# Kernel optimization log

Hardware: AMD Instinct MI355X
Metric: run time of the kernel (lower is better)

The kernel has to match this reference:

```python
import jax, jax.numpy as jnp
import numpy as np

B, S, D, K = 8, 4096, 256, 8192
BETA = 0.25


def setup_inputs() -> dict:
    key = jax.random.key(0)
    k1, k2 = jax.random.split(key)
    return {
        "z": jax.random.normal(k1, (B, S, D), dtype=jnp.float32),
        "embed": jax.random.normal(k2, (K, D), dtype=jnp.float32),
    }


def reference(z, embed):
    # Inference-path VQ-EMA forward (EMA buffer updates are a no-grad side
    # effect only active in training mode; excluded from the pure reference).
    num_codes, dim = embed.shape
    z_flat = z.reshape(-1, dim)                      # [N, D]
    # squared-euclidean distances: ||z||^2 - 2 z.e^T + ||e||^2  -> [N, K]
    dist = ((z_flat * z_flat).sum(1, keepdims=True)
            - 2.0 * (z_flat @ embed.T)
            + (embed * embed).sum(1)[None, :])
    idx = jnp.argmin(dist, axis=1)                   # [N]
    z_q = embed[idx].reshape(z.shape)                # gather instead of onehot @ embed
    # commitment loss: beta * mse(stop_grad(z_q), z)
    loss = BETA * jnp.mean(jnp.square(jax.lax.stop_gradient(z_q) - z))
    # straight-through estimator
    z_q_st = z + jax.lax.stop_gradient(z_q - z)
    # perplexity from code usage histogram (scatter-add instead of onehot.mean)
    counts = jnp.zeros((num_codes,), dtype=z.dtype).at[idx].add(1.0)
    avg_probs = counts / idx.shape[0]
    perplexity = jnp.exp(-jnp.sum(avg_probs * jnp.log(avg_probs + 1e-12)))
    return z_q_st, loss, perplexity, idx.reshape(z.shape[:-1])
```

## Files before the change

### kernel.cpp

```cpp
#include <hip/hip_runtime.h>
#include <stdint.h>
#include <math.h>

#define NROWS 32768
#define DIM   256
#define KCODES 8192
#define BETA  0.25f
#define CSPLIT 4
#define RSPLIT 16
#define NELEM 8388608
#define TAU 0.09375f

typedef float f32x4 __attribute__((ext_vector_type(4)));
typedef _Float16 v8h __attribute__((ext_vector_type(8)));
typedef unsigned short us4 __attribute__((ext_vector_type(4)));

__device__ inline unsigned int split1(float x) {
    _Float16 hf = (_Float16)x;
    _Float16 lf = (_Float16)(x - (float)hf);
    unsigned int h = __builtin_bit_cast(unsigned short, hf);
    unsigned int l = __builtin_bit_cast(unsigned short, lf);
    return h | (l << 16);
}

__device__ inline void gload_lds16(const void* g, void* l) {
    __builtin_amdgcn_global_load_lds(
        (const __attribute__((address_space(1))) void*)g,
        (__attribute__((address_space(3))) void*)l,
        16, 0, 0);
}

__device__ inline unsigned int fkey(float f) {
    unsigned int b = __float_as_uint(f);
    return (b & 0x80000000u) ? ~b : (b | 0x80000000u);
}

__global__ void prep_z(const float* __restrict__ z,
                       unsigned short* __restrict__ zhi,
                       unsigned short* __restrict__ zlo) {
    int t = blockIdx.x * blockDim.x + threadIdx.x;
    float4 v = reinterpret_cast<const float4*>(z)[t];
    unsigned int p0 = split1(v.x);
    unsigned int p1 = split1(v.y);
    unsigned int p2 = split1(v.z);
    unsigned int p3 = split1(v.w);
    us4 h, l;
    h[0] = (unsigned short)p0; l[0] = (unsigned short)(p0 >> 16);
    h[1] = (unsigned short)p1; l[1] = (unsigned short)(p1 >> 16);
    h[2] = (unsigned short)p2; l[2] = (unsigned short)(p2 >> 16);
    h[3] = (unsigned short)p3; l[3] = (unsigned short)(p3 >> 16);
    reinterpret_cast<us4*>(zhi)[t] = h;
    reinterpret_cast<us4*>(zlo)[t] = l;
}

__global__ void prep_e(const float* __restrict__ e,
                       unsigned short* __restrict__ ehi,
                       unsigned short* __restrict__ elo,
                       float* __restrict__ enrm) {
    int row = blockIdx.x;
    int d = threadIdx.x;
    float x = e[(size_t)row * DIM + d];
    unsigned int p = split1(x);
    ehi[(size_t)row * DIM + d] = (unsigned short)p;
    elo[(size_t)row * DIM + d] = (unsigned short)(p >> 16);
    float sq = x * x;
    #pragma unroll
    for (int off = 32; off; off >>= 1) sq += __shfl_down(sq, off);
    __shared__ float ps[4];
    if ((threadIdx.x & 63) == 0) ps[threadIdx.x >> 6] = sq;
    __syncthreads();
    if (threadIdx.x == 0) enrm[row] = 0.5f * (ps[0] + ps[1] + ps[2] + ps[3]);
}

__launch_bounds__(256, 2)
__global__ void gemm_hi(const unsigned short* __restrict__ zhi,
                        const unsigned short* __restrict__ ehi,
                        const float* __restrict__ enrm,
                        float* __restrict__ pval1,
                        int* __restrict__ pcol1,
                        float* __restrict__ pval2) {
    __shared__ __align__(16) unsigned short As[128 * 64];
    __shared__ __align__(16) unsigned short Bs[128 * 64];
    __shared__ float rv[2][128];
    __shared__ int   rc[2][128];
    __shared__ float rv2[2][128];

    const int tid = threadIdx.x;
    const int w = tid >> 6, l = tid & 63;
    const int lx = l & 15, quad = l >> 4;
    const int wm = w >> 1, wn = w & 1;
    const int arow_base = blockIdx.x * 128;
    const int cs = blockIdx.y;
    const int cbase_cs = cs * (KCODES / CSPLIT);

    float runv[16], runv2[16];
    int runc[16];
    #pragma unroll
    for (int s = 0; s < 16; ++s) {
        runv[s] = 3.0e38f; runv2[s] = 3.0e38f; runc[s] = 0x7fffffff;
    }

    const int st_row8 = l >> 3;
    const int st_g = (((l & 7) ^ (l >> 3)) * 8);
    const int fr_lx7 = lx & 7;

    for (int nt = 0; nt < (KCODES / CSPLIT) / 128; ++nt) {
        const int colbase = cbase_cs + nt * 128;
        f32x4 acc[4][4];
        #pragma unroll
        for (int mi = 0; mi < 4; ++mi)
            #pragma unroll
            for (int ni = 0; ni < 4; ++ni) {
                f32x4 zz = {0.f, 0.f, 0.f, 0.f};
                acc[mi][ni] = zz;
            }

        for (int bk = 0; bk < 4; ++bk) {
            const int ao = bk * 64;
            __syncthreads();
            #pragma unroll
            for (int j = 0; j < 4; ++j) {
                const int r = w * 32 + j * 8 + st_row8;
                gload_lds16(zhi + (size_t)(arow_base + r) * DIM + ao + st_g,
                            &As[(w * 32 + j * 8) * 64]);
                gload_lds16(ehi + (size_t)(colbase + r) * DIM + ao + st_g,
                            &Bs[(w * 32 + j * 8) * 64]);
            }
            __syncthreads();

            #pragma unroll
            for (int kc = 0; kc < 2; ++kc) {
                const int gsw = ((kc * 4 + quad) ^ fr_lx7) * 8;
                v8h af[4], bfr[4];
                #pragma unroll
                for (int mi = 0; mi < 4; ++mi)
                    af[mi] = *(const v8h*)&As[(wm * 64 + mi * 16 + lx) * 64 + gsw];
                #pragma unroll
                for (int ni = 0; ni < 4; ++ni)
                    bfr[ni] = *(const v8h*)&Bs[(wn * 64 + ni * 16 + lx) * 64 + gsw];
                #pragma unroll
                for (int mi = 0; mi < 4; ++mi)
                    #pragma unroll
                    for (int ni = 0; ni < 4; ++ni)
                        acc[mi][ni] = __builtin_amdgcn_mfma_f32_16x16x32_f16(
                            af[mi], bfr[ni], acc[mi][ni], 0, 0, 0);
            }
        }

        #pragma unroll
        for (int ni = 0; ni < 4; ++ni) {
            const int col = colbase + wn * 64 + ni * 16 + lx;
            const float es = enrm[col];
            #pragma unroll
            for (int mi = 0; mi < 4; ++mi)
                #pragma unroll
                for (int r = 0; r < 4; ++r) {
                    const int s = mi * 4 + r;
                    float sv = es - acc[mi][ni][r];
                    bool lt1 = sv < runv[s];
                    bool lt2 = sv < runv2[s];
                    float old1 = runv[s];
                    runv2[s] = lt1 ? old1 : (lt2 ? sv : runv2[s]);
                    runv[s] = lt1 ? sv : old1;
                    runc[s] = lt1 ? col : runc[s];
                }
        }
    }

    #pragma unroll
    for (int s = 0; s < 16; ++s) {
        float v1 = runv[s], v2 = runv2[s];
        int c1 = runc[s];
        #pragma unroll
        for (int m = 1; m < 16; m <<= 1) {
            float ov1 = __shfl_xor(v1, m);
            int oc1 = __shfl_xor(c1, m);
            float ov2 = __shfl_xor(v2, m);
            float mx = fmaxf(v1, ov1);
            v2 = fminf(fminf(v2, ov2), mx);
            bool take = (ov1 < v1) || (ov1 == v1 && oc1 < c1);
            v1 = take ? ov1 : v1;
            c1 = take ? oc1 : c1;
        }
        if (lx == 0) {
            const int mi = s >> 2, r = s & 3;
            const int rl = wm * 64 + mi * 16 + quad * 4 + r;
            rv[wn][rl] = v1; rc[wn][rl] = c1; rv2[wn][rl] = v2;
        }
    }
    __syncthreads();
    if (tid < 128) {
        float v1 = rv[0][tid], v2 = rv2[0][tid];
        int c1 = rc[0][tid];
        float ov1 = rv[1][tid], ov2 = rv2[1][tid];
        int oc1 = rc[1][tid];
        float mx = fmaxf(v1, ov1);
        v2 = fminf(fminf(v2, ov2), mx);
        bool take = (ov1 < v1) || (ov1 == v1 && oc1 < c1);
        v1 = take ? ov1 : v1;
        c1 = take ? oc1 : c1;
        const size_t row = (size_t)arow_base + tid;
        pval1[row * CSPLIT + cs] = v1;
        pcol1[row * CSPLIT + cs] = c1;
        pval2[row * CSPLIT + cs] = v2;
    }
}

__global__ void merge_flag(const float* __restrict__ pval1,
                           const int* __restrict__ pcol1,
                           const float* __restrict__ pval2,
                           int* __restrict__ colidx,
                           float* __restrict__ out_idx,
                           int* __restrict__ flagcnt,
                           int* __restrict__ flaglist) {
    int row = blockIdx.x * blockDim.x + threadIdx.x;
    float v1 = pval1[row * CSPLIT], v2 = pval2[row * CSPLIT];
    int c1 = pcol1[row * CSPLIT];
    #pragma unroll
    for (int cs = 1; cs < CSPLIT; ++cs) {
        float ov1 = pval1[row * CSPLIT + cs], ov2 = pval2[row * CSPLIT + cs];
        int oc1 = pcol1[row * CSPLIT + cs];
        float mx = fmaxf(v1, ov1);
        v2 = fminf(fminf(v2, ov2), mx);
        if (ov1 < v1 || (ov1 == v1 && oc1 < c1)) { v1 = ov1; c1 = oc1; }
    }
    colidx[row] = c1;
    out_idx[row] = (float)c1;
    if (v2 - v1 < TAU) {
        int slot = atomicAdd(flagcnt, 1);
        flaglist[slot] = row;
    }
}

__launch_bounds__(256, 2)
__global__ void rescue_gemm(const unsigned short* __restrict__ zhi,
                            const unsigned short* __restrict__ zlo,
                            const unsigned short* __restrict__ ehi,
                            const unsigned short* __restrict__ elo,
                            const float* __restrict__ enrm,
                            const int* __restrict__ flagcnt,
                            const int* __restrict__ flaglist,
                            unsigned long long* __restrict__ rkey) {
    __shared__ __align__(16) unsigned short As[128 * 64];
    __shared__ __align__(16) unsigned short Bs[128 * 64];
    __shared__ float rv[2][128];
    __shared__ int   rc[2][128];

    const int count = *flagcnt;
    const int tid = threadIdx.x;
    const int w = tid >> 6, l = tid & 63;
    const int lx = l & 15, quad = l >> 4;
    const int wm = w >> 1, wn = w & 1;
    const int cs = blockIdx.y;
    const int cbase_cs = cs * (KCODES / RSPLIT);

    const int st_row8 = l >> 3;
    const int st_g = (((l & 7) ^ (l >> 3)) * 8);
    const int fr_lx7 = lx & 7;

    for (int tb = blockIdx.x * 128; tb < count; tb += 32 * 128) {
        int arowj[4];
        #pragma unroll
        for (int j = 0; j < 4; ++j) {
            int li = tb + w * 32 + j * 8 + st_row8;
            arowj[j] = (li < count) ? flaglist[li] : 0;
        }

        float runv[16];
        int runc[16];
        #pragma unroll
        for (int s = 0; s < 16; ++s) { runv[s] = 3.0e38f; runc[s] = 0x7fffffff; }

        for (int nt = 0; nt < (KCODES / RSPLIT) / 128; ++nt) {
            const int colbase = cbase_cs + nt * 128;
            f32x4 acc[4][4];
            #pragma unroll
            for (int mi = 0; mi < 4; ++mi)
                #pragma unroll
                for (int ni = 0; ni < 4; ++ni) {
                    f32x4 zz = {0.f, 0.f, 0.f, 0.f};
                    acc[mi][ni] = zz;
                }

            #pragma unroll
            for (int seg = 0; seg < 3; ++seg) {
                const unsigned short* za = (seg == 2) ? zlo : zhi;
                const unsigned short* eb = (seg == 1) ? elo : ehi;
                for (int bk = 0; bk < 4; ++bk) {
                    const int ao = bk * 64;
                    __syncthreads();
                    #pragma unroll
                    for (int j = 0; j < 4; ++j) {
                        const int r = w * 32 + j * 8 + st_row8;
                        gload_lds16(za + (size_t)arowj[j] * DIM + ao + st_g,
                                    &As[(w * 32 + j * 8) * 64]);
                        gload_lds16(eb + (size_t)(colbase + r) * DIM + ao + st_g,
                                    &Bs[(w * 32 + j * 8) * 64]);
                    }
                    __syncthreads();
                    #pragma unroll
                    for (int kc = 0; kc < 2; ++kc) {
                        const int gsw = ((kc * 4 + quad) ^ fr_lx7) * 8;
                        v8h af[4], bfr[4];
                        #pragma unroll
                        for (int mi = 0; mi < 4; ++mi)
                            af[mi] = *(const v8h*)&As[(wm * 64 + mi * 16 + lx) * 64 + gsw];
                        #pragma unroll
                        for (int ni = 0; ni < 4; ++ni)
                            bfr[ni] = *(const v8h*)&Bs[(wn * 64 + ni * 16 + lx) * 64 + gsw];
                        #pragma unroll
                        for (int mi = 0; mi < 4; ++mi)
                            #pragma unroll
                            for (int ni = 0; ni < 4; ++ni)
                                acc[mi][ni] = __builtin_amdgcn_mfma_f32_16x16x32_f16(
                                    af[mi], bfr[ni], acc[mi][ni], 0, 0, 0);
                    }
                }
            }

            #pragma unroll
            for (int ni = 0; ni < 4; ++ni) {
                const int col = colbase + wn * 64 + ni * 16 + lx;
                const float es = enrm[col];
                #pragma unroll
                for (int mi = 0; mi < 4; ++mi)
                    #pragma unroll
                    for (int r = 0; r < 4; ++r) {
                        float sv = es - acc[mi][ni][r];
                        const int s = mi * 4 + r;
                        if (sv < runv[s]) { runv[s] = sv; runc[s] = col; }
                    }
            }
        }

        #pragma unroll
        for (int s = 0; s < 16; ++s) {
            float v = runv[s]; int c = runc[s];
            #pragma unroll
            for (int m = 1; m < 16; m <<= 1) {
                float ov = __shfl_xor(v, m);
                int oc = __shfl_xor(c, m);
                if (ov < v || (ov == v && oc < c)) { v = ov; c = oc; }
            }
            if (lx == 0) {
                const int mi = s >> 2, r = s & 3;
                const int rl = wm * 64 + mi * 16 + quad * 4 + r;
                rv[wn][rl] = v; rc[wn][rl] = c;
            }
        }
        __syncthreads();
        if (tid < 128) {
            float v0 = rv[0][tid]; int c0 = rc[0][tid];
            float v1 = rv[1][tid]; int c1 = rc[1][tid];
            if (v1 < v0 || (v1 == v0 && c1 < c0)) { v0 = v1; c0 = c1; }
            const int li = tb + tid;
            if (li < count) {
                unsigned long long key =
                    ((unsigned long long)fkey(v0) << 32) | (unsigned int)c0;
                atomicMin(&rkey[li], key);
            }
        }
        __syncthreads();
    }
}

__global__ void rescue_write(const unsigned long long* __restrict__ rkey,
                             const int* __restrict__ flagcnt,
                             const int* __restrict__ flaglist,
                             int* __restrict__ colidx,
                             float* __restrict__ out_idx) {
    int i = blockIdx.x * blockDim.x + threadIdx.x;
    if (i >= *flagcnt) return;
    int row = flaglist[i];
    int col = (int)(unsigned int)(rkey[i] & 0xFFFFFFFFull);
    colidx[row] = col;
    out_idx[row] = (float)col;
}

__global__ void fused_out(const int* __restrict__ colidx,
                          const float* __restrict__ z,
                          const float* __restrict__ embed,
                          float* __restrict__ out_zq,
                          float* __restrict__ counts,
                          float* __restrict__ lossAcc) {
    __shared__ int cidx[16];
    const int tid = threadIdx.x;
    if (tid < 16) {
        const int row = blockIdx.x * 16 + tid;
        const int c = colidx[row];
        cidx[tid] = c;
        atomicAdd(&counts[c], 1.0f);
    }
    __syncthreads();
    const int d = tid;
    float ls = 0.f;
    #pragma unroll 4
    for (int i = 0; i < 16; ++i) {
        const int row = blockIdx.x * 16 + i;
        const int c = cidx[i];
        const float zv = z[(size_t)row * DIM + d];
        const float ev = embed[(size_t)c * DIM + d];
        const float diff = ev - zv;
        out_zq[(size_t)row * DIM + d] = zv + diff;
        ls += diff * diff;
    }
    #pragma unroll
    for (int off = 32; off; off >>= 1) ls += __shfl_down(ls, off);
    __shared__ float ps[4];
    if ((tid & 63) == 0) ps[tid >> 6] = ls;
    __syncthreads();
    if (tid == 0) atomicAdd(lossAcc, ps[0] + ps[1] + ps[2] + ps[3]);
}

__global__ void finalize(const float* __restrict__ counts,
                         const float* __restrict__ lossAcc,
                         float* __restrict__ out_loss,
                         float* __restrict__ out_perp) {
    float h = 0.f;
    for (int k = threadIdx.x; k < KCODES; k += 256) {
        float p = counts[k] * (1.0f / (float)NROWS);
        h += p * logf(p + 1e-12f);
    }
    #pragma unroll
    for (int off = 32; off; off >>= 1) h += __shfl_down(h, off);
    __shared__ float ps[4];
    if ((threadIdx.x & 63) == 0) ps[threadIdx.x >> 6] = h;
    __syncthreads();
    if (threadIdx.x == 0) {
        *out_perp = expf(-(ps[0] + ps[1] + ps[2] + ps[3]));
        *out_loss = BETA * lossAcc[0] / (float)NELEM;
    }
}

extern "C" void kernel_launch(void* const* d_in, const int* in_sizes, int n_in,
                              void* d_out, int out_size, void* d_ws, size_t ws_size,
                              hipStream_t stream) {
    const float* z = (const float*)d_in[0];
    const float* embed = (const float*)d_in[1];
    char* ws = (char*)d_ws;

    unsigned short* zhi = (unsigned short*)(ws + 0);
    unsigned short* zlo = (unsigned short*)(ws + 16777216);
    unsigned short* ehi = (unsigned short*)(ws + 33554432);
    unsigned short* elo = (unsigned short*)(ws + 37748736);
    float* enrm    = (float*)(ws + 41943040);
    float* pval1   = (float*)(ws + 41975808);
    int*   pcol1   = (int*)  (ws + 42500096);
    float* pval2   = (float*)(ws + 43024384);
    int*   colidx  = (int*)  (ws + 43548672);
    float* counts  = (float*)(ws + 43679744);
    float* lossAcc = (float*)(ws + 43712512);
    int*   flagcnt = (int*)  (ws + 43712516);
    int*   flaglist = (int*) (ws + 43712520);
    unsigned long long* rkey = (unsigned long long*)(ws + 43843592);

    float* out = (float*)d_out;
    float* out_zq   = out;
    float* out_loss = out + 8388608;
    float* out_perp = out + 8388609;
    float* out_idx  = out + 8388610;

    (void)hipMemsetAsync(counts, 0, KCODES * 4 + 8, stream);
    (void)hipMemsetAsync(rkey, 0xFF, NROWS * 8, stream);

    prep_z<<<NELEM / 4 / 256, 256, 0, stream>>>(z, zhi, zlo);
    prep_e<<<KCODES, 256, 0, stream>>>(embed, ehi, elo, enrm);
    gemm_hi<<<dim3(NROWS / 128, CSPLIT), 256, 0, stream>>>(
        zhi, ehi, enrm, pval1, pcol1, pval2);
    merge_flag<<<NROWS / 256, 256, 0, stream>>>(
        pval1, pcol1, pval2, colidx, out_idx, flagcnt, flaglist);
    rescue_gemm<<<dim3(32, RSPLIT), 256, 0, stream>>>(
        zhi, zlo, ehi, elo, enrm, flagcnt, flaglist, rkey);
    rescue_write<<<NROWS / 256, 256, 0, stream>>>(
        rkey, flagcnt, flaglist, colidx, out_idx);
    fused_out<<<NROWS / 16, 256, 0, stream>>>(colidx, z, embed,
                                              out_zq, counts, lossAcc);
    finalize<<<1, 256, 0, stream>>>(counts, lossAcc, out_loss, out_perp);
}
```

Measured before the change: 387.0 us.

## Merge prep kernels, drop memsets and rescue_write, use med3 for top-2 tracking

Fuses prep_z and prep_e into one launch that also zeroes counts, the loss accumulator and the flag counter, which removes both memsets. rkey is now initialised per flagged slot in merge_flag, and flagged rows store a negative slot reference in colidx. fused_out resolves that reference, so the separate rescue_write kernel goes away. The top-2 update in gemm_hi uses fmed3/fminf instead of selects to cut VALU work in the inner epilogue. The hot epilogue's tie handling changes slightly, since fminf and the strict less-than comparison are used together.

```diff
diff --git a/kernel.cpp b/kernel.cpp
--- a/kernel.cpp
+++ b/kernel.cpp
@@ -35,41 +35,49 @@
     return (b & 0x80000000u) ? ~b : (b | 0x80000000u);
 }
 
-__global__ void prep_z(const float* __restrict__ z,
-                       unsigned short* __restrict__ zhi,
-                       unsigned short* __restrict__ zlo) {
-    int t = blockIdx.x * blockDim.x + threadIdx.x;
-    float4 v = reinterpret_cast<const float4*>(z)[t];
-    unsigned int p0 = split1(v.x);
-    unsigned int p1 = split1(v.y);
-    unsigned int p2 = split1(v.z);
-    unsigned int p3 = split1(v.w);
-    us4 h, l;
-    h[0] = (unsigned short)p0; l[0] = (unsigned short)(p0 >> 16);
-    h[1] = (unsigned short)p1; l[1] = (unsigned short)(p1 >> 16);
-    h[2] = (unsigned short)p2; l[2] = (unsigned short)(p2 >> 16);
-    h[3] = (unsigned short)p3; l[3] = (unsigned short)(p3 >> 16);
-    reinterpret_cast<us4*>(zhi)[t] = h;
-    reinterpret_cast<us4*>(zlo)[t] = l;
-}
-
-__global__ void prep_e(const float* __restrict__ e,
-                       unsigned short* __restrict__ ehi,
-                       unsigned short* __restrict__ elo,
-                       float* __restrict__ enrm) {
-    int row = blockIdx.x;
-    int d = threadIdx.x;
-    float x = e[(size_t)row * DIM + d];
-    unsigned int p = split1(x);
-    ehi[(size_t)row * DIM + d] = (unsigned short)p;
-    elo[(size_t)row * DIM + d] = (unsigned short)(p >> 16);
-    float sq = x * x;
-    #pragma unroll
-    for (int off = 32; off; off >>= 1) sq += __shfl_down(sq, off);
-    __shared__ float ps[4];
-    if ((threadIdx.x & 63) == 0) ps[threadIdx.x >> 6] = sq;
-    __syncthreads();
-    if (threadIdx.x == 0) enrm[row] = 0.5f * (ps[0] + ps[1] + ps[2] + ps[3]);
+__global__ void prep_all(const float* __restrict__ z,
+                         const float* __restrict__ e,
+                         unsigned short* __restrict__ zhi,
+                         unsigned short* __restrict__ zlo,
+                         unsigned short* __restrict__ ehi,
+                         unsigned short* __restrict__ elo,
+                         float* __restrict__ enrm,
+                         float* __restrict__ counts,
+                         float* __restrict__ lossAcc,
+                         int* __restrict__ flagcnt) {
+    if (blockIdx.x < 8192) {
+        int t = blockIdx.x * 256 + threadIdx.x;
+        float4 v = reinterpret_cast<const float4*>(z)[t];
+        unsigned int p0 = split1(v.x);
+        unsigned int p1 = split1(v.y);
+        unsigned int p2 = split1(v.z);
+        unsigned int p3 = split1(v.w);
+        us4 h, l;
+        h[0] = (unsigned short)p0; l[0] = (unsigned short)(p0 >> 16);
+        h[1] = (unsigned short)p1; l[1] = (unsigned short)(p1 >> 16);
+        h[2] = (unsigned short)p2; l[2] = (unsigned short)(p2 >> 16);
+        h[3] = (unsigned short)p3; l[3] = (unsigned short)(p3 >> 16);
+        reinterpret_cast<us4*>(zhi)[t] = h;
+        reinterpret_cast<us4*>(zlo)[t] = l;
+    } else {
+        int row = blockIdx.x - 8192;
+        int d = threadIdx.x;
+        float x = e[(size_t)row * DIM + d];
+        unsigned int p = split1(x);
+        ehi[(size_t)row * DIM + d] = (unsigned short)p;
+        elo[(size_t)row * DIM + d] = (unsigned short)(p >> 16);
+        float sq = x * x;
+        #pragma unroll
+        for (int off = 32; off; off >>= 1) sq += __shfl_down(sq, off);
+        __shared__ float ps[4];
+        if ((threadIdx.x & 63) == 0) ps[threadIdx.x >> 6] = sq;
+        __syncthreads();
+        if (threadIdx.x == 0) {
+            enrm[row] = 0.5f * (ps[0] + ps[1] + ps[2] + ps[3]);
+            counts[row] = 0.f;
+            if (row == 0) { *lossAcc = 0.f; *flagcnt = 0; }
+        }
+    }
 }
 
 __launch_bounds__(256, 2)
@@ -157,12 +165,10 @@
                 for (int r = 0; r < 4; ++r) {
                     const int s = mi * 4 + r;
                     float sv = es - acc[mi][ni][r];
-                    bool lt1 = sv < runv[s];
-                    bool lt2 = sv < runv2[s];
-                    float old1 = runv[s];
-                    runv2[s] = lt1 ? old1 : (lt2 ? sv : runv2[s]);
-                    runv[s] = lt1 ? sv : old1;
-                    runc[s] = lt1 ? col : runc[s];
+                    bool lt = sv < runv[s];
+                    runv2[s] = __builtin_amdgcn_fmed3f(sv, runv[s], runv2[s]);
+                    runc[s] = lt ? col : runc[s];
+                    runv[s] = fminf(runv[s], sv);
                 }
         }
     }
@@ -212,7 +218,8 @@
                            int* __restrict__ colidx,
                            float* __restrict__ out_idx,
                            int* __restrict__ flagcnt,
-                           int* __restrict__ flaglist) {
+                           int* __restrict__ flaglist,
+                           unsigned long long* __restrict__ rkey) {
     int row = blockIdx.x * blockDim.x + threadIdx.x;
     float v1 = pval1[row * CSPLIT], v2 = pval2[row * CSPLIT];
     int c1 = pcol1[row * CSPLIT];
@@ -224,11 +231,14 @@
         v2 = fminf(fminf(v2, ov2), mx);
         if (ov1 < v1 || (ov1 == v1 && oc1 < c1)) { v1 = ov1; c1 = oc1; }
     }
-    colidx[row] = c1;
     out_idx[row] = (float)c1;
     if (v2 - v1 < TAU) {
         int slot = atomicAdd(flagcnt, 1);
         flaglist[slot] = row;
+        rkey[slot] = ~0ull;
+        colidx[row] = -(slot + 1);
+    } else {
+        colidx[row] = c1;
     }
 }
 
@@ -364,30 +374,23 @@
     }
 }
 
-__global__ void rescue_write(const unsigned long long* __restrict__ rkey,
-                             const int* __restrict__ flagcnt,
-                             const int* __restrict__ flaglist,
-                             int* __restrict__ colidx,
-                             float* __restrict__ out_idx) {
-    int i = blockIdx.x * blockDim.x + threadIdx.x;
-    if (i >= *flagcnt) return;
-    int row = flaglist[i];
-    int col = (int)(unsigned int)(rkey[i] & 0xFFFFFFFFull);
-    colidx[row] = col;
-    out_idx[row] = (float)col;
-}
-
 __global__ void fused_out(const int* __restrict__ colidx,
+                          const unsigned long long* __restrict__ rkey,
                           const float* __restrict__ z,
                           const float* __restrict__ embed,
                           float* __restrict__ out_zq,
+                          float* __restrict__ out_idx,
                           float* __restrict__ counts,
                           float* __restrict__ lossAcc) {
     __shared__ int cidx[16];
     const int tid = threadIdx.x;
     if (tid < 16) {
         const int row = blockIdx.x * 16 + tid;
-        const int c = colidx[row];
+        int c = colidx[row];
+        if (c < 0) {
+            c = (int)(unsigned int)(rkey[-c - 1] & 0x1FFFull);
+            out_idx[row] = (float)c;
+        }
         cidx[tid] = c;
         atomicAdd(&counts[c], 1.0f);
     }
@@ -460,20 +463,15 @@
     float* out_perp = out + 8388609;
     float* out_idx  = out + 8388610;
 
-    (void)hipMemsetAsync(counts, 0, KCODES * 4 + 8, stream);
-    (void)hipMemsetAsync(rkey, 0xFF, NROWS * 8, stream);
-
-    prep_z<<<NELEM / 4 / 256, 256, 0, stream>>>(z, zhi, zlo);
-    prep_e<<<KCODES, 256, 0, stream>>>(embed, ehi, elo, enrm);
+    prep_all<<<16384, 256, 0, stream>>>(z, embed, zhi, zlo, ehi, elo, enrm,
+                                        counts, lossAcc, flagcnt);
     gemm_hi<<<dim3(NROWS / 128, CSPLIT), 256, 0, stream>>>(
         zhi, ehi, enrm, pval1, pcol1, pval2);
     merge_flag<<<NROWS / 256, 256, 0, stream>>>(
-        pval1, pcol1, pval2, colidx, out_idx, flagcnt, flaglist);
+        pval1, pcol1, pval2, colidx, out_idx, flagcnt, flaglist, rkey);
     rescue_gemm<<<dim3(32, RSPLIT), 256, 0, stream>>>(
         zhi, zlo, ehi, elo, enrm, flagcnt, flaglist, rkey);
-    rescue_write<<<NROWS / 256, 256, 0, stream>>>(
-        rkey, flagcnt, flaglist, colidx, out_idx);
-    fused_out<<<NROWS / 16, 256, 0, stream>>>(colidx, z, embed,
-                                              out_zq, counts, lossAcc);
+    fused_out<<<NROWS / 16, 256, 0, stream>>>(colidx, rkey, z, embed,
+                                              out_zq, out_idx, counts, lossAcc);
     finalize<<<1, 256, 0, stream>>>(counts, lossAcc, out_loss, out_perp);
 }
```

Result: faster. 368.2 us (-4.9%).
